# Performance work log

Measured on AMD Instinct MI355X. Metric: run time of the kernel, lower is better.

## Reference

```python
import jax, jax.numpy as jnp
import numpy as np

N = 2_097_152  # total atoms
G = 32_768     # number of graphs (~64 atoms each)
EPS = 1e-4     # sign-detection threshold from the original code


def setup_inputs() -> dict:
    key = jax.random.key(0)
    k1, k2 = jax.random.split(key)
    pos = jax.random.normal(k1, (N, 3), dtype=jnp.float32) * 3.0
    batch = jnp.sort(jax.random.randint(k2, (N,), 0, G))
    return {"pos": pos, "batch": batch, "num_graphs": G}


def reference(pos, batch, num_graphs):
    n = pos.shape[0]
    dtype = pos.dtype

    # per-graph centroid (scatter_mean)
    counts = jax.ops.segment_sum(jnp.ones((n,), dtype), batch, num_segments=num_graphs)
    center = jax.ops.segment_sum(pos, batch, num_segments=num_graphs) / jnp.maximum(counts, 1.0)[:, None]
    pc = pos - center[batch]                      # [N,3] centered positions

    # per-atom inertia contribution: r^2 * I - p p^T, then scatter_add per graph
    r_sq = jnp.sum(pc * pc, axis=-1)              # [N]
    outer = jnp.einsum('ni,nj->nij', pc, pc)      # [N,3,3]
    I_atom = r_sq[:, None, None] * jnp.eye(3, dtype=dtype) - outer
    I_mol = jax.ops.segment_sum(I_atom, batch, num_segments=num_graphs)  # [G,3,3]

    L, Q = jnp.linalg.eigh(I_mol)                 # Q: [G,3,3], columns = principal axes

    # projections of centered positions onto the (pre-flip) eigenbasis.
    # NOTE: in the torch loop, p_proj is computed once before any sign flips, and
    # flipping column 0 does not affect p_proj[:,1], so axes 0 and 1 are independent.
    proj = jnp.einsum('ni,nij->nj', pc, Q[batch])  # [N,3]

    idx = jnp.arange(n)

    def axis_sign(a):
        # parallel "first atom (in original order) with |proj| > EPS" per graph
        qual = jnp.abs(proj[:, a]) > EPS
        key_idx = jnp.where(qual, idx, n)
        first = jax.ops.segment_min(key_idx, batch, num_segments=num_graphs)  # [G]
        found = first < n
        val = proj[jnp.minimum(first, n - 1), a]
        return jnp.where(found & (val < 0), -1.0, 1.0).astype(dtype)

    s0 = axis_sign(0)
    s1 = axis_sign(1)
    q0 = Q[:, :, 0] * s0[:, None]
    q1 = Q[:, :, 1] * s1[:, None]
    q2 = jnp.cross(q0, q1)  # enforce right-handed frame
    return jnp.stack([q0, q1, q2], axis=-1)       # [G,3,3]
```

## Files before the change

kernel.cpp:

```cpp
#include <hip/hip_runtime.h>
#include <math.h>

#define CANON_EPS 1e-4f

__global__ __launch_bounds__(256) void build_starts_kernel(
    const int* __restrict__ batch, int* __restrict__ wsi, int n, int G) {
  int t = (int)(blockIdx.x * (unsigned)blockDim.x + threadIdx.x);
  int base = t * 4;
  if (base >= n) return;

  int b0, b1, b2, b3;
  if (base + 4 <= n) {
    int4 b4 = *reinterpret_cast<const int4*>(batch + base);
    b0 = b4.x; b1 = b4.y; b2 = b4.z; b3 = b4.w;
  } else {
    b0 = batch[base];
    b1 = (base + 1 < n) ? batch[base + 1] : b0;
    b2 = (base + 2 < n) ? batch[base + 2] : b1;
    b3 = (base + 3 < n) ? batch[base + 3] : b2;
  }
  int bp = (base > 0) ? batch[base - 1] : -1;

  int B[4] = {b0, b1, b2, b3};
#pragma unroll
  for (int j = 0; j < 4; ++j) {
    int i = base + j;
    if (i >= n) break;
    int prev = (j == 0) ? bp : B[j - 1];
    int b = B[j];
    for (int g = prev + 1; g <= b; ++g) wsi[g] = i;
    if (i == n - 1) {
      for (int g = b + 1; g <= G; ++g) wsi[g] = n;
    }
  }
}

__device__ __forceinline__ void jacobi3_f32(float a00, float a11, float a22,
                                            float a01, float a02, float a12,
                                            float Q[3][3]) {
  float A00 = a00, A11 = a11, A22 = a22;
  float A01 = a01, A02 = a02, A12 = a12;
  float Q00 = 1.f, Q01 = 0.f, Q02 = 0.f;
  float Q10 = 0.f, Q11 = 1.f, Q12 = 0.f;
  float Q20 = 0.f, Q21 = 0.f, Q22 = 1.f;

#define ROT(App, Aqq, Apq, Akp, Akq, Qrp0, Qrq0, Qrp1, Qrq1, Qrp2, Qrq2)     \
  {                                                                          \
    float apq = Apq;                                                         \
    float theta = (Aqq - App) / (2.0f * apq);                                \
    float t = copysignf(1.0f, theta) /                                       \
              (fabsf(theta) + sqrtf(1.0f + theta * theta));                  \
    t = (apq == 0.0f) ? 0.0f : t;                    \
    float c = 1.0f / sqrtf(1.0f + t * t);                                    \
    float s = t * c;                                                         \
    App = App - t * apq;                                                     \
    Aqq = Aqq + t * apq;                                                     \
    Apq = 0.0f;                                                              \
    float akp = Akp, akq = Akq;                                              \
    Akp = c * akp - s * akq;                                                 \
    Akq = s * akp + c * akq;                                                 \
    float r0p = Qrp0, r0q = Qrq0;                                            \
    Qrp0 = c * r0p - s * r0q;                                                \
    Qrq0 = s * r0p + c * r0q;                                                \
    float r1p = Qrp1, r1q = Qrq1;                                            \
    Qrp1 = c * r1p - s * r1q;                                                \
    Qrq1 = s * r1p + c * r1q;                                                \
    float r2p = Qrp2, r2q = Qrq2;                                            \
    Qrp2 = c * r2p - s * r2q;                                                \
    Qrq2 = s * r2p + c * r2q;                                                \
  }

#pragma unroll
  for (int sweep = 0; sweep < 4; ++sweep) {
    ROT(A00, A11, A01, A02, A12, Q00, Q01, Q10, Q11, Q20, Q21);
    ROT(A00, A22, A02, A01, A12, Q00, Q02, Q10, Q12, Q20, Q22);
    ROT(A11, A22, A12, A01, A02, Q01, Q02, Q11, Q12, Q21, Q22);
  }
#undef ROT

  float w0 = A00, w1 = A11, w2 = A22;
#define CSWAP(wa, wb, qa0, qb0, qa1, qb1, qa2, qb2)                          \
  {                                                                          \
    bool sw = (wb) < (wa);                                                   \
    float tw = wa; wa = sw ? wb : wa; wb = sw ? tw : wb;                     \
    float t0 = qa0; qa0 = sw ? qb0 : qa0; qb0 = sw ? t0 : qb0;               \
    float t1 = qa1; qa1 = sw ? qb1 : qa1; qb1 = sw ? t1 : qb1;               \
    float t2 = qa2; qa2 = sw ? qb2 : qa2; qb2 = sw ? t2 : qb2;               \
  }
  CSWAP(w0, w1, Q00, Q01, Q10, Q11, Q20, Q21);
  CSWAP(w1, w2, Q01, Q02, Q11, Q12, Q21, Q22);
  CSWAP(w0, w1, Q00, Q01, Q10, Q11, Q20, Q21);
#undef CSWAP

  Q[0][0] = Q00; Q[0][1] = Q01; Q[0][2] = Q02;
  Q[1][0] = Q10; Q[1][1] = Q11; Q[1][2] = Q12;
  Q[2][0] = Q20; Q[2][1] = Q21; Q[2][2] = Q22;
}

__global__ __launch_bounds__(256) void fused_kernel(
    const float* __restrict__ pos, const int* __restrict__ wsi,
    float* __restrict__ out, int G) {
  __shared__ float lmom[16][9];
  __shared__ float latm[16][12];
  __shared__ int lsc[16][2];

  int tid = (int)threadIdx.x;
  int lg = tid >> 4;
  int sub = tid & 15;
  int gid = (int)blockIdx.x * 16 + lg;
  bool gv = gid < G;

  int s = 0, e = 0;
  if (gv) {
    s = wsi[gid];
    e = wsi[gid + 1];
  }
  int cnt = e - s;

  float sx = 0.f, sy = 0.f, sz = 0.f;
  float sxx = 0.f, syy = 0.f, szz = 0.f, sxy = 0.f, sxz = 0.f, syz = 0.f;
  float r0x = 0.f, r0y = 0.f, r0z = 0.f;

#pragma unroll
  for (int k = 0; k < 5; ++k) {
    int i = s + sub + 16 * k;
    bool in = i < e;
    int ii = in ? i : 0;
    float rx = pos[3 * ii + 0];
    float ry = pos[3 * ii + 1];
    float rz = pos[3 * ii + 2];
    if (k == 0) { r0x = rx; r0y = ry; r0z = rz; }
    float m = in ? 1.0f : 0.0f;
    float x = rx * m, y = ry * m, z = rz * m;
    sx += x; sy += y; sz += z;
    sxx = fmaf(x, x, sxx); syy = fmaf(y, y, syy); szz = fmaf(z, z, szz);
    sxy = fmaf(x, y, sxy); sxz = fmaf(x, z, sxz); syz = fmaf(y, z, syz);
  }
  for (int i = s + 80 + sub; i < e; i += 16) {
    float x = pos[3 * i + 0];
    float y = pos[3 * i + 1];
    float z = pos[3 * i + 2];
    sx += x; sy += y; sz += z;
    sxx = fmaf(x, x, sxx); syy = fmaf(y, y, syy); szz = fmaf(z, z, szz);
    sxy = fmaf(x, y, sxy); sxz = fmaf(x, z, sxz); syz = fmaf(y, z, syz);
  }

#define RED16(v)                                                             \
  v += __shfl_xor(v, 1); v += __shfl_xor(v, 2);                              \
  v += __shfl_xor(v, 4); v += __shfl_xor(v, 8);
  RED16(sx) RED16(sy) RED16(sz)
  RED16(sxx) RED16(syy) RED16(szz)
  RED16(sxy) RED16(sxz) RED16(syz)
#undef RED16

  if (sub < 4 && gv) {
    latm[lg][3 * sub + 0] = r0x;
    latm[lg][3 * sub + 1] = r0y;
    latm[lg][3 * sub + 2] = r0z;
  }
  if (sub == 0 && gv) {
    float fn = (float)(cnt > 0 ? cnt : 1);
    float inv = 1.0f / fn;
    float mx = sx * inv, my = sy * inv, mz = sz * inv;
    float Sxx = fmaf(-fn * mx, mx, sxx);
    float Syy = fmaf(-fn * my, my, syy);
    float Szz = fmaf(-fn * mz, mz, szz);
    float Sxy = fmaf(-fn * mx, my, sxy);
    float Sxz = fmaf(-fn * mx, mz, sxz);
    float Syz = fmaf(-fn * my, mz, syz);
    lmom[lg][0] = mx; lmom[lg][1] = my; lmom[lg][2] = mz;
    lmom[lg][3] = Syy + Szz;
    lmom[lg][4] = Sxx + Szz;
    lmom[lg][5] = Sxx + Syy;
    lmom[lg][6] = -Sxy;
    lmom[lg][7] = -Sxz;
    lmom[lg][8] = -Syz;
    lsc[lg][0] = s; lsc[lg][1] = cnt;
  }
  __syncthreads();

  if (tid < 16) {
    int g = (int)blockIdx.x * 16 + tid;
    if (g < G) {
      float cx = lmom[tid][0], cy = lmom[tid][1], cz = lmom[tid][2];
      float Q[3][3];
      jacobi3_f32(lmom[tid][3], lmom[tid][4], lmom[tid][5], lmom[tid][6],
                  lmom[tid][7], lmom[tid][8], Q);

      float q00 = Q[0][0], q10 = Q[1][0], q20 = Q[2][0];
      float q01 = Q[0][1], q11 = Q[1][1], q21 = Q[2][1];

      int s2 = lsc[tid][0];
      int cnt2 = lsc[tid][1];

      bool found0 = false, found1 = false;
      float v0s = 0.f, v1s = 0.f;
#define CHECK(J)                                                             \
  if ((J) < cnt2) {                                                          \
    float x = latm[tid][3 * (J) + 0] - cx;                                   \
    float y = latm[tid][3 * (J) + 1] - cy;                                   \
    float z = latm[tid][3 * (J) + 2] - cz;                                   \
    float p0 = x * q00 + y * q10 + z * q20;                                  \
    float p1 = x * q01 + y * q11 + z * q21;                                  \
    if (!found0 && fabsf(p0) > CANON_EPS) { v0s = p0; found0 = true; }       \
    if (!found1 && fabsf(p1) > CANON_EPS) { v1s = p1; found1 = true; }       \
  }
      CHECK(0) CHECK(1) CHECK(2) CHECK(3)
#undef CHECK
      for (int i = s2 + 4; i < s2 + cnt2 && !(found0 && found1); ++i) {
        float x = pos[3 * i + 0] - cx;
        float y = pos[3 * i + 1] - cy;
        float z = pos[3 * i + 2] - cz;
        float p0 = x * q00 + y * q10 + z * q20;
        float p1 = x * q01 + y * q11 + z * q21;
        if (!found0 && fabsf(p0) > CANON_EPS) { v0s = p0; found0 = true; }
        if (!found1 && fabsf(p1) > CANON_EPS) { v1s = p1; found1 = true; }
      }
      float s0 = (found0 && v0s < 0.f) ? -1.f : 1.f;
      float s1 = (found1 && v1s < 0.f) ? -1.f : 1.f;

      float q0x = q00 * s0, q0y = q10 * s0, q0z = q20 * s0;
      float q1x = q01 * s1, q1y = q11 * s1, q1z = q21 * s1;
      float q2x = q0y * q1z - q0z * q1y;
      float q2y = q0z * q1x - q0x * q1z;
      float q2z = q0x * q1y - q0y * q1x;
      float* o = out + (size_t)g * 9;
      o[0] = q0x; o[1] = q1x; o[2] = q2x;
      o[3] = q0y; o[4] = q1y; o[5] = q2y;
      o[6] = q0z; o[7] = q1z; o[8] = q2z;
    }
  }
}

extern "C" void kernel_launch(void* const* d_in, const int* in_sizes, int n_in,
                              void* d_out, int out_size, void* d_ws, size_t ws_size,
                              hipStream_t stream) {
  const float* pos = (const float*)d_in[0];
  const int* batch = (const int*)d_in[1];
  float* out = (float*)d_out;

  int n = in_sizes[0] / 3;
  int G = out_size / 9;

  int* wsi = (int*)d_ws;

  int t1 = (n + 3) / 4;
  build_starts_kernel<<<(t1 + 255) / 256, 256, 0, stream>>>(batch, wsi, n, G);

  fused_kernel<<<(G + 15) / 16, 256, 0, stream>>>(pos, wsi, out, G);
}
```

Before: 22.06 us.

## Replace segment-start prefix kernel with in-kernel 8-ary ballot binary search

Removes the separate kernel that scanned the sorted batch array to build per-graph start offsets. Each 16-thread group instead finds its graph's start and end with a cooperative 8-way search over the sorted batch array, using wave ballots, inside the main kernel. This cuts one launch and a full pass over the batch array, at the cost of about eight rounds of dependent scattered loads before the per-graph work begins.

```diff
diff --git a/kernel.cpp b/kernel.cpp
--- a/kernel.cpp
+++ b/kernel.cpp
@@ -2,38 +2,6 @@
 #include <math.h>
 
 #define CANON_EPS 1e-4f
-
-__global__ __launch_bounds__(256) void build_starts_kernel(
-    const int* __restrict__ batch, int* __restrict__ wsi, int n, int G) {
-  int t = (int)(blockIdx.x * (unsigned)blockDim.x + threadIdx.x);
-  int base = t * 4;
-  if (base >= n) return;
-
-  int b0, b1, b2, b3;
-  if (base + 4 <= n) {
-    int4 b4 = *reinterpret_cast<const int4*>(batch + base);
-    b0 = b4.x; b1 = b4.y; b2 = b4.z; b3 = b4.w;
-  } else {
-    b0 = batch[base];
-    b1 = (base + 1 < n) ? batch[base + 1] : b0;
-    b2 = (base + 2 < n) ? batch[base + 2] : b1;
-    b3 = (base + 3 < n) ? batch[base + 3] : b2;
-  }
-  int bp = (base > 0) ? batch[base - 1] : -1;
-
-  int B[4] = {b0, b1, b2, b3};
-#pragma unroll
-  for (int j = 0; j < 4; ++j) {
-    int i = base + j;
-    if (i >= n) break;
-    int prev = (j == 0) ? bp : B[j - 1];
-    int b = B[j];
-    for (int g = prev + 1; g <= b; ++g) wsi[g] = i;
-    if (i == n - 1) {
-      for (int g = b + 1; g <= G; ++g) wsi[g] = n;
-    }
-  }
-}
 
 __device__ __forceinline__ void jacobi3_f32(float a00, float a11, float a22,
                                             float a01, float a02, float a12,
@@ -97,9 +65,9 @@
   Q[2][0] = Q20; Q[2][1] = Q21; Q[2][2] = Q22;
 }
 
-__global__ __launch_bounds__(256) void fused_kernel(
-    const float* __restrict__ pos, const int* __restrict__ wsi,
-    float* __restrict__ out, int G) {
+__global__ __launch_bounds__(256) void canon_all_kernel(
+    const float* __restrict__ pos, const int* __restrict__ batch,
+    float* __restrict__ out, int n, int G) {
   __shared__ float lmom[16][9];
   __shared__ float latm[16][12];
   __shared__ int lsc[16][2];
@@ -107,14 +75,40 @@
   int tid = (int)threadIdx.x;
   int lg = tid >> 4;
   int sub = tid & 15;
+  int lane = tid & 63;
   int gid = (int)blockIdx.x * 16 + lg;
   bool gv = gid < G;
 
-  int s = 0, e = 0;
-  if (gv) {
-    s = wsi[gid];
-    e = wsi[gid + 1];
-  }
+  int t0 = gv ? gid : (G - 1);
+  int half = (lane >> 3) & 1;
+  int tgt = t0 + half;
+  int j = lane & 7;
+  int base = lane & 0x30;
+
+  int r = 1;
+  while (r < n) r <<= 3;
+  int lo0 = 0, lo1 = 0;
+  while (r > 1) {
+    int step = r >> 3;
+    int myLo = half ? lo1 : lo0;
+    int m = myLo + j * step;
+    int mm = m - 1;
+    mm = mm < 0 ? 0 : (mm > n - 1 ? n - 1 : mm);
+    bool c = (j == 0) || ((m <= n) && (batch[mm] < tgt));
+    unsigned long long b = __ballot(c);
+    unsigned c0 = (unsigned)((b >> base) & 0xFEull);
+    unsigned c1 = (unsigned)((b >> (base + 8)) & 0xFEull);
+    lo0 += __popc(c0) * step;
+    lo1 += __popc(c1) * step;
+    r = step;
+  }
+  {
+    int i0 = lo0 < n - 1 ? lo0 : n - 1;
+    int i1 = lo1 < n - 1 ? lo1 : n - 1;
+    lo0 += ((lo0 < n) && (batch[i0] < t0)) ? 1 : 0;
+    lo1 += ((lo1 < n) && (batch[i1] < t0 + 1)) ? 1 : 0;
+  }
+  int s = lo0, e = lo1;
   int cnt = e - s;
 
   float sx = 0.f, sy = 0.f, sz = 0.f;
@@ -242,10 +236,5 @@
   int n = in_sizes[0] / 3;
   int G = out_size / 9;
 
-  int* wsi = (int*)d_ws;
-
-  int t1 = (n + 3) / 4;
-  build_starts_kernel<<<(t1 + 255) / 256, 256, 0, stream>>>(batch, wsi, n, G);
-
-  fused_kernel<<<(G + 15) / 16, 256, 0, stream>>>(pos, wsi, out, G);
+  canon_all_kernel<<<(G + 15) / 16, 256, 0, stream>>>(pos, batch, out, n, G);
 }
```

After: 21.10 us, median of 2. -4.3%, faster.
